# Kernel optimization log

Hardware: AMD Instinct MI355X
Metric: run time of the kernel (lower is better)

## Reference

```python
import jax, jax.numpy as jnp
import numpy as np

B = 8
H = W = 1280
STRIDES = (8, 16, 32)
TOP_K = 5000
CONF_TH = 0.3
NMS_TH = 0.3
KEEP_TOP_K = 750
NUM_KPS = 5


def _make_priors():
    # Mirrors _PriorBox: per feature cell [x, y, stride, stride] in pixels, offset=0,
    # x varies fastest (torch repeat pattern == row-major meshgrid 'xy').
    pts = []
    for s in STRIDES:
        fh, fw = H // s, W // s
        xs = np.arange(fw, dtype=np.float32) * s
        ys = np.arange(fh, dtype=np.float32) * s
        xx, yy = np.meshgrid(xs, ys)  # [fh, fw]
        p = np.stack([xx.ravel(), yy.ravel(),
                      np.full(fh * fw, s, np.float32),
                      np.full(fh * fw, s, np.float32)], axis=1)
        pts.append(p)
    return jnp.asarray(np.concatenate(pts, axis=0))  # [N, 4]


def setup_inputs() -> dict:
    key = jax.random.key(0)
    k1, k2, k3, k4 = jax.random.split(key, 4)
    priors = _make_priors()
    N = priors.shape[0]  # 33600
    return {
        'cls_preds': jax.random.uniform(k1, (B, N, 1), dtype=jnp.float32),
        'obj_preds': jax.random.uniform(k2, (B, N, 1), dtype=jnp.float32),
        'bbox_preds': jax.random.normal(k3, (B, N, 4), dtype=jnp.float32),
        'kps_preds': jax.random.normal(k4, (B, N, 2 * NUM_KPS), dtype=jnp.float32),
        'priors': priors,
    }


def _decode(bbox_preds, kps_preds, priors):
    # Faithful port of _decode with scale=1 (priors already in pixel units).
    pxy = priors[:, :2]   # [N,2]
    pwh = priors[:, 2:4]  # [N,2]
    cxy = pxy + bbox_preds[..., 0:2] * pwh                 # [B,N,2] box center
    wh = pwh * jnp.exp(bbox_preds[..., 2:4])               # [B,N,2] box size
    Bn, N = bbox_preds.shape[:2]
    kps = pxy[:, None, :] + kps_preds.reshape(Bn, N, NUM_KPS, 2) * pwh[:, None, :]
    x1y1 = cxy - wh * 0.5
    return jnp.concatenate([x1y1, x1y1 + wh, kps.reshape(Bn, N, 2 * NUM_KPS)], axis=-1)  # [B,N,14]


def _nms_keep(boxes, valid):
    # boxes: [K,4] xyxy sorted by score desc; valid: [K] bool. Greedy NMS keep mask.
    b = jax.lax.stop_gradient(boxes)
    area = jnp.maximum(b[:, 2] - b[:, 0], 0.0) * jnp.maximum(b[:, 3] - b[:, 1], 0.0)
    lt = jnp.maximum(b[:, None, :2], b[None, :, :2])
    rb = jnp.minimum(b[:, None, 2:], b[None, :, 2:])
    whi = jnp.maximum(rb - lt, 0.0)
    inter = whi[..., 0] * whi[..., 1]                      # [K,K]
    iou = inter / (area[:, None] + area[None, :] - inter + 1e-12)
    K = b.shape[0]
    jidx = jnp.arange(K)

    def body(i, keep):
        sup = keep[i] & (iou[i] > NMS_TH) & (jidx > i)
        return keep & ~sup

    return jax.lax.fori_loop(0, K, body, valid)


def reference(cls_preds, obj_preds, bbox_preds, kps_preds, priors):
    boxes = _decode(bbox_preds, kps_preds, priors)          # [B,N,14]
    scores = jnp.sqrt(cls_preds[..., 0] * obj_preds[..., 0])  # [B,N] geometric-mean score

    # confidence filter + pre-NMS top-k (masked scores sort invalids last)
    masked = jnp.where(scores > CONF_TH, scores, -1.0)
    top_scores, idx = jax.lax.top_k(masked, TOP_K)          # [B,K]
    top_boxes = jnp.take_along_axis(boxes, idx[..., None], axis=1)  # [B,K,14]
    valid = top_scores > CONF_TH

    keep = jax.lax.stop_gradient(jax.vmap(_nms_keep)(top_boxes[..., :4], valid))  # [B,K]

    dets = jnp.concatenate([top_boxes, top_scores[..., None]], axis=-1)  # [B,K,15]
    kept_scores = jnp.where(keep, top_scores, -1.0)
    fs, fidx = jax.lax.top_k(kept_scores, KEEP_TOP_K)
    out = jnp.take_along_axis(dets, fidx[..., None], axis=1)  # [B,750,15]
    out_valid = fs > CONF_TH                                   # [B,750]
    return out, out_valid
```

## Files before the change

kernel.cpp:

```cpp
#include <hip/hip_runtime.h>
#include <stdint.h>

#pragma clang fp contract(off)

static constexpr int TOPK  = 5000;
static constexpr int KEEPK = 750;
static constexpr int MPAD  = 65536;
static constexpr int NBLK  = (TOPK + 63) / 64;
static constexpr int KROW  = NBLK * 64;
static constexpr float TH  = 0.3f;

__device__ __forceinline__ uint32_t key_of(float f) {
  uint32_t u = __float_as_uint(f);
  u = (u & 0x80000000u) ? ~u : (u | 0x80000000u);
  return ~u;
}
__device__ __forceinline__ float val_of(uint32_t key) {
  uint32_t u = ~key;
  return (u & 0x80000000u) ? __uint_as_float(u ^ 0x80000000u) : __uint_as_float(~u);
}

__global__ void build_keys(const float* __restrict__ cls, const float* __restrict__ obj,
                           uint64_t* __restrict__ keys, int N) {
  int b = blockIdx.y;
  int i = blockIdx.x * blockDim.x + threadIdx.x;
  if (i >= MPAD) return;
  uint64_t c = ~0ull;
  if (i < N) {
    size_t o = (size_t)b * N + i;
    float s = sqrtf(cls[o] * obj[o]);
    float m = (s > TH) ? s : -1.0f;
    c = ((uint64_t)key_of(m) << 32) | (uint32_t)i;
  }
  keys[(size_t)b * MPAD + i] = c;
}

__global__ __launch_bounds__(1024) void bitonic_local_full(uint64_t* __restrict__ keys) {
  __shared__ uint64_t sh[8192];
  int base = blockIdx.x * 8192;
  uint64_t* a = keys + (size_t)blockIdx.y * MPAD + base;
  for (int t = threadIdx.x; t < 8192; t += 1024) sh[t] = a[t];
  __syncthreads();
  for (int k = 2; k <= 8192; k <<= 1) {
    for (int j = k >> 1; j > 0; j >>= 1) {
      for (int t = threadIdx.x; t < 4096; t += 1024) {
        int i = ((t & ~(j - 1)) << 1) | (t & (j - 1));
        int l = i | j;
        bool asc = (((base + i) & k) == 0);
        uint64_t x = sh[i], y = sh[l];
        if ((x > y) == asc) { sh[i] = y; sh[l] = x; }
      }
      __syncthreads();
    }
  }
  for (int t = threadIdx.x; t < 8192; t += 1024) a[t] = sh[t];
}

__global__ __launch_bounds__(1024) void merge_prune(const uint64_t* __restrict__ src,
                                                    uint64_t* __restrict__ dst) {
  __shared__ uint64_t sh[8192];
  int m = blockIdx.x, b = blockIdx.y;
  const uint64_t* A  = src + ((size_t)b * gridDim.x * 2 + 2 * m) * 8192;
  const uint64_t* Bp = A + 8192;
  for (int t = threadIdx.x; t < 8192; t += 1024) {
    uint64_t x = A[t], y = Bp[t];
    sh[t] = x < y ? x : y;
  }
  __syncthreads();
  bool asc = ((m & 1) == 0);
  for (int j = 4096; j > 0; j >>= 1) {
    for (int t = threadIdx.x; t < 4096; t += 1024) {
      int i = ((t & ~(j - 1)) << 1) | (t & (j - 1));
      int l = i | j;
      uint64_t x = sh[i], y = sh[l];
      if ((x > y) == asc) { sh[i] = y; sh[l] = x; }
    }
    __syncthreads();
  }
  uint64_t* D = dst + ((size_t)b * gridDim.x + m) * 8192;
  for (int t = threadIdx.x; t < 8192; t += 1024) D[t] = sh[t];
}

__global__ void gather_decode(const uint64_t* __restrict__ keys,
                              const float* __restrict__ bbox, const float* __restrict__ kps,
                              const float* __restrict__ priors,
                              float* __restrict__ dets, float* __restrict__ tscore, int N) {
  int b = blockIdx.y;
  int r = blockIdx.x * blockDim.x + threadIdx.x;
  if (r >= TOPK) return;
  uint64_t c = keys[(size_t)b * 8192 + r];
  uint32_t idx = (uint32_t)c;
  float score = val_of((uint32_t)(c >> 32));
  float4 pr = ((const float4*)priors)[idx];
  const float* bb = bbox + ((size_t)b * N + idx) * 4;
  float cx = pr.x + bb[0] * pr.z;
  float cy = pr.y + bb[1] * pr.w;
  float w = pr.z * expf(bb[2]);
  float h = pr.w * expf(bb[3]);
  float x1 = cx - w * 0.5f, y1 = cy - h * 0.5f;
  float* d = dets + ((size_t)b * TOPK + r) * 16;
  d[0] = x1; d[1] = y1; d[2] = x1 + w; d[3] = y1 + h;
  const float* kp = kps + ((size_t)b * N + idx) * 10;
#pragma unroll
  for (int q = 0; q < 5; ++q) {
    d[4 + 2 * q] = pr.x + kp[2 * q] * pr.z;
    d[5 + 2 * q] = pr.y + kp[2 * q + 1] * pr.w;
  }
  d[14] = score;
  tscore[(size_t)b * TOPK + r] = score;
}

__global__ __launch_bounds__(64) void nms_mask(const float* __restrict__ dets,
                                               uint64_t* __restrict__ tmask) {
  int sbk = blockIdx.x, tbk = blockIdx.y, b = blockIdx.z;
  if (tbk < sbk) return;
  __shared__ float4 tbox[64];
  int t = threadIdx.x;
  int j0 = tbk * 64;
  {
    int j = j0 + t;
    if (j < TOPK) {
      const float* dj = dets + ((size_t)b * TOPK + j) * 16;
      tbox[t] = make_float4(dj[0], dj[1], dj[2], dj[3]);
    } else tbox[t] = make_float4(0.f, 0.f, 0.f, 0.f);
  }
  __syncthreads();
  int i = sbk * 64 + t;
  uint64_t bits = 0;
  if (i < TOPK) {
    const float* di = dets + ((size_t)b * TOPK + i) * 16;
    float ix1 = di[0], iy1 = di[1], ix2 = di[2], iy2 = di[3];
    float iar = fmaxf(ix2 - ix1, 0.f) * fmaxf(iy2 - iy1, 0.f);
    int jmax = min(64, TOPK - j0);
    for (int u = 0; u < jmax; ++u) {
      int j = j0 + u;
      if (j <= i) continue;
      float4 bx = tbox[u];
      float xx1 = fmaxf(ix1, bx.x), yy1 = fmaxf(iy1, bx.y);
      float xx2 = fminf(ix2, bx.z), yy2 = fminf(iy2, bx.w);
      float ww = fmaxf(xx2 - xx1, 0.f), hh = fmaxf(yy2 - yy1, 0.f);
      float inter = ww * hh;
      float jar = fmaxf(bx.z - bx.x, 0.f) * fmaxf(bx.w - bx.y, 0.f);
      float iou = inter / (iar + jar - inter + 1e-12f);
      if (iou > TH) bits |= (1ull << u);
    }
  }
  uint64_t tw = 0;
#pragma unroll
  for (int u = 0; u < 64; ++u) {
    uint64_t bal = __ballot((bits >> u) & 1ull);
    if (t == u) tw = bal;
  }
  tmask[((size_t)b * NBLK + tbk) * KROW + (size_t)(sbk * 64 + t)] = tw;
}

__global__ __launch_bounds__(1024) void nms_fix_emit(const uint64_t* __restrict__ tmask,
                                                     const float* __restrict__ tscore,
                                                     const float* __restrict__ dets,
                                                     float* __restrict__ out, int B) {
  __shared__ uint64_t s_keep[2][80];
  __shared__ int s_changed;
  __shared__ int s_pref[NBLK + 1];
  int b = blockIdx.x;
  int tid = threadIdx.x;
  int wid = tid >> 6, lane = tid & 63;
  const uint64_t* mb = tmask + (size_t)b * NBLK * KROW;
  const float* sb = tscore + (size_t)b * TOPK;

  float sc[5];
  bool val[5];
#pragma unroll
  for (int q = 0; q < 5; ++q) {
    int j = tid + q * 1024;
    sc[q] = (j < TOPK) ? sb[j] : -1.0f;
    val[q] = (j < TOPK) && (sc[q] > TH);
  }
#pragma unroll
  for (int q = 0; q < 5; ++q) {
    uint64_t w = __ballot(val[q]);
    int ch = wid + q * 16;
    if (ch < NBLK && lane == 0) s_keep[0][ch] = w;
  }

  int cur = 0;
  for (;;) {
    __syncthreads();
    if (tid == 0) s_changed = 0;
    __syncthreads();
    const uint64_t* kp = s_keep[cur];
#pragma unroll
    for (int q = 0; q < 5; ++q) {
      int j = tid + q * 1024;
      int tc = j >> 6;
      uint64_t sup = 0;
      if (tc < NBLK) {
        const uint64_t* row = mb + (size_t)tc * KROW + lane;
        uint64_t a0 = 0, a1 = 0, a2 = 0, a3 = 0;
        int nw = tc + 1, w = 0;
        for (; w + 4 <= nw; w += 4) {
          uint64_t m0 = row[(w + 0) * 64], m1 = row[(w + 1) * 64];
          uint64_t m2 = row[(w + 2) * 64], m3 = row[(w + 3) * 64];
          a0 |= m0 & kp[w + 0]; a1 |= m1 & kp[w + 1];
          a2 |= m2 & kp[w + 2]; a3 |= m3 & kp[w + 3];
        }
        for (; w < nw; ++w) a0 |= row[w * 64] & kp[w];
        sup = (a0 | a1) | (a2 | a3);
      }
      uint64_t nk = __ballot(val[q] && sup == 0);
      int ch = wid + q * 16;
      if (ch < NBLK && lane == 0) {
        s_keep[cur ^ 1][ch] = nk;
        if (nk != kp[ch]) s_changed = 1;
      }
    }
    __syncthreads();
    if (!s_changed) break;
    cur ^= 1;
  }

  if (tid == 0) {
    int run = 0;
    for (int cb = 0; cb < NBLK; ++cb) { s_pref[cb] = run; run += __popcll(s_keep[cur][cb]); }
    s_pref[NBLK] = run;
  }
  __syncthreads();
  int K = s_pref[NBLK];

  for (int cb = wid; cb < NBLK; cb += 16) {
    int p = cb * 64 + lane;
    if (p >= TOPK) continue;
    uint64_t aw = s_keep[cur][cb];
    int kept = (int)((aw >> lane) & 1ull);
    int within = __popcll(aw & ((1ull << lane) - 1ull));
    int rank = s_pref[cb] + within;
    int slot = kept ? rank : (K + (p - s_pref[cb] - within));
    if (slot < KEEPK) {
      const float* d = dets + ((size_t)b * TOPK + p) * 16;
      float* o = out + ((size_t)b * KEEPK + slot) * 15;
#pragma unroll
      for (int ccol = 0; ccol < 15; ++ccol) o[ccol] = d[ccol];
      out[(size_t)B * KEEPK * 15 + (size_t)b * KEEPK + slot] = kept ? 1.0f : 0.0f;
    }
  }
}

extern "C" void kernel_launch(void* const* d_in, const int* in_sizes, int n_in,
                              void* d_out, int out_size, void* d_ws, size_t ws_size,
                              hipStream_t stream) {
  const float* cls    = (const float*)d_in[0];
  const float* obj    = (const float*)d_in[1];
  const float* bbox   = (const float*)d_in[2];
  const float* kps    = (const float*)d_in[3];
  const float* priors = (const float*)d_in[4];
  int N = in_sizes[4] / 4;
  int B = in_sizes[0] / N;
  if (N > MPAD) return;

  char* ws = (char*)d_ws;
  size_t off = 0;
  auto alloc = [&](size_t bytes) -> void* {
    void* p = ws + off;
    off += (bytes + 255) & ~(size_t)255;
    return p;
  };
  uint64_t* keys1  = (uint64_t*)alloc((size_t)B * MPAD * 8);
  float*    dets   = (float*)   alloc((size_t)B * TOPK * 16 * 4);
  float*    tscore = (float*)   alloc((size_t)B * TOPK * 4 + 4096);
  uint64_t* tmask  = (uint64_t*)alloc((size_t)B * NBLK * KROW * 8 + 4096);
  if (off > ws_size) return;
  uint64_t* keys2 = tmask;
  uint64_t* keys3 = keys2 + (size_t)B * 4 * 8192;
  uint64_t* keys4 = keys3 + (size_t)B * 2 * 8192;

  build_keys<<<dim3((MPAD + 255) / 256, B), 256, 0, stream>>>(cls, obj, keys1, N);
  bitonic_local_full<<<dim3(MPAD / 8192, B), 1024, 0, stream>>>(keys1);
  merge_prune<<<dim3(4, B), 1024, 0, stream>>>(keys1, keys2);
  merge_prune<<<dim3(2, B), 1024, 0, stream>>>(keys2, keys3);
  merge_prune<<<dim3(1, B), 1024, 0, stream>>>(keys3, keys4);
  gather_decode<<<dim3((TOPK + 255) / 256, B), 256, 0, stream>>>(keys4, bbox, kps, priors,
                                                                 dets, tscore, N);
  nms_mask<<<dim3(NBLK, NBLK, B), 64, 0, stream>>>(dets, tmask);
  nms_fix_emit<<<B, 1024, 0, stream>>>(tmask, tscore, dets, (float*)d_out, B);
}
```

Baseline: 377.5 us.

## Restructure NMS mask kernel: triangular grid, transposed loop, division-free IoU test

Launches only the upper-triangular block pairs through a linear pair index, so the grid no longer spawns blocks that exit immediately. Each thread now owns a target box and loops over source boxes held in shared memory, which produces the transposed mask word directly and removes the 64-step ballot transpose. The IoU threshold test becomes a multiply-compare against precomputed areas written by gather_decode, with an exact-division fallback for near-ties to keep bit-exactness. It costs an extra areas buffer, some integer sqrt math per block, and a slightly more complex diagonal mask.

After: 329.9 us. -12.6%, faster.

```diff
diff --git a/kernel.cpp b/kernel.cpp
--- a/kernel.cpp
+++ b/kernel.cpp
@@ -7,6 +7,7 @@
 static constexpr int KEEPK = 750;
 static constexpr int MPAD  = 65536;
 static constexpr int NBLK  = (TOPK + 63) / 64;
+static constexpr int NPAIR = NBLK * (NBLK + 1) / 2;
 static constexpr int KROW  = NBLK * 64;
 static constexpr float TH  = 0.3f;
 
@@ -84,7 +85,8 @@
 __global__ void gather_decode(const uint64_t* __restrict__ keys,
                               const float* __restrict__ bbox, const float* __restrict__ kps,
                               const float* __restrict__ priors,
-                              float* __restrict__ dets, float* __restrict__ tscore, int N) {
+                              float* __restrict__ dets, float* __restrict__ tscore,
+                              float* __restrict__ areas, int N) {
   int b = blockIdx.y;
   int r = blockIdx.x * blockDim.x + threadIdx.x;
   if (r >= TOPK) return;
@@ -98,8 +100,10 @@
   float w = pr.z * expf(bb[2]);
   float h = pr.w * expf(bb[3]);
   float x1 = cx - w * 0.5f, y1 = cy - h * 0.5f;
+  float x2 = x1 + w, y2 = y1 + h;
   float* d = dets + ((size_t)b * TOPK + r) * 16;
-  d[0] = x1; d[1] = y1; d[2] = x1 + w; d[3] = y1 + h;
+  d[0] = x1; d[1] = y1; d[2] = x2; d[3] = y2;
+  areas[(size_t)b * TOPK + r] = fmaxf(x2 - x1, 0.0f) * fmaxf(y2 - y1, 0.0f);
   const float* kp = kps + ((size_t)b * N + idx) * 10;
 #pragma unroll
   for (int q = 0; q < 5; ++q) {
@@ -111,46 +115,58 @@
 }
 
 __global__ __launch_bounds__(64) void nms_mask(const float* __restrict__ dets,
+                                               const float* __restrict__ areas,
                                                uint64_t* __restrict__ tmask) {
-  int sbk = blockIdx.x, tbk = blockIdx.y, b = blockIdx.z;
-  if (tbk < sbk) return;
-  __shared__ float4 tbox[64];
+  int pid = blockIdx.x, b = blockIdx.y;
+  int tbk = (int)((sqrtf(8.0f * (float)pid + 1.0f) - 1.0f) * 0.5f);
+  while (((tbk + 1) * (tbk + 2)) / 2 <= pid) ++tbk;
+  while ((tbk * (tbk + 1)) / 2 > pid) --tbk;
+  int sbk = pid - (tbk * (tbk + 1)) / 2;
+
+  __shared__ float4 sbox[64];
+  __shared__ float sarea[64];
   int t = threadIdx.x;
-  int j0 = tbk * 64;
   {
-    int j = j0 + t;
-    if (j < TOPK) {
-      const float* dj = dets + ((size_t)b * TOPK + j) * 16;
-      tbox[t] = make_float4(dj[0], dj[1], dj[2], dj[3]);
-    } else tbox[t] = make_float4(0.f, 0.f, 0.f, 0.f);
+    int i = min(sbk * 64 + t, TOPK - 1);
+    const float* di = dets + ((size_t)b * TOPK + i) * 16;
+    sbox[t] = make_float4(di[0], di[1], di[2], di[3]);
+    sarea[t] = areas[(size_t)b * TOPK + i];
   }
   __syncthreads();
-  int i = sbk * 64 + t;
-  uint64_t bits = 0;
-  if (i < TOPK) {
-    const float* di = dets + ((size_t)b * TOPK + i) * 16;
-    float ix1 = di[0], iy1 = di[1], ix2 = di[2], iy2 = di[3];
-    float iar = fmaxf(ix2 - ix1, 0.f) * fmaxf(iy2 - iy1, 0.f);
-    int jmax = min(64, TOPK - j0);
-    for (int u = 0; u < jmax; ++u) {
-      int j = j0 + u;
-      if (j <= i) continue;
-      float4 bx = tbox[u];
-      float xx1 = fmaxf(ix1, bx.x), yy1 = fmaxf(iy1, bx.y);
-      float xx2 = fminf(ix2, bx.z), yy2 = fminf(iy2, bx.w);
+
+  int jc = min(tbk * 64 + t, TOPK - 1);
+  const float* dj = dets + ((size_t)b * TOPK + jc) * 16;
+  float jx1 = dj[0], jy1 = dj[1], jx2 = dj[2], jy2 = dj[3];
+  float ja = areas[(size_t)b * TOPK + jc];
+
+  uint64_t tw = 0, unc = 0;
+#pragma unroll
+  for (int u = 0; u < 64; ++u) {
+    float4 bx = sbox[u];
+    float xx1 = fmaxf(jx1, bx.x), yy1 = fmaxf(jy1, bx.y);
+    float xx2 = fminf(jx2, bx.z), yy2 = fminf(jy2, bx.w);
+    float ww = fmaxf(xx2 - xx1, 0.f), hh = fmaxf(yy2 - yy1, 0.f);
+    float inter = ww * hh;
+    float denom = sarea[u] + ja - inter + 1e-12f;
+    float rhs = TH * denom;
+    tw  |= (uint64_t)(inter > rhs) << u;
+    unc |= (uint64_t)(fabsf(inter - rhs) <= 6e-7f * rhs) << u;
+  }
+  if (unc) {
+    do {
+      int u = __ffsll((unsigned long long)unc) - 1;
+      float4 bx = sbox[u];
+      float xx1 = fmaxf(jx1, bx.x), yy1 = fmaxf(jy1, bx.y);
+      float xx2 = fminf(jx2, bx.z), yy2 = fminf(jy2, bx.w);
       float ww = fmaxf(xx2 - xx1, 0.f), hh = fmaxf(yy2 - yy1, 0.f);
       float inter = ww * hh;
-      float jar = fmaxf(bx.z - bx.x, 0.f) * fmaxf(bx.w - bx.y, 0.f);
-      float iou = inter / (iar + jar - inter + 1e-12f);
-      if (iou > TH) bits |= (1ull << u);
-    }
-  }
-  uint64_t tw = 0;
-#pragma unroll
-  for (int u = 0; u < 64; ++u) {
-    uint64_t bal = __ballot((bits >> u) & 1ull);
-    if (t == u) tw = bal;
-  }
+      float denom = sarea[u] + ja - inter + 1e-12f;
+      uint64_t bit = 1ull << u;
+      tw = (tw & ~bit) | ((inter / denom > TH) ? bit : 0ull);
+      unc &= unc - 1;
+    } while (unc);
+  }
+  if (sbk == tbk) tw &= (t == 0) ? 0ull : ((1ull << t) - 1ull);
   tmask[((size_t)b * NBLK + tbk) * KROW + (size_t)(sbk * 64 + t)] = tw;
 }
 
@@ -266,6 +282,7 @@
   uint64_t* keys1  = (uint64_t*)alloc((size_t)B * MPAD * 8);
   float*    dets   = (float*)   alloc((size_t)B * TOPK * 16 * 4);
   float*    tscore = (float*)   alloc((size_t)B * TOPK * 4 + 4096);
+  float*    areas  = (float*)   alloc((size_t)B * TOPK * 4 + 4096);
   uint64_t* tmask  = (uint64_t*)alloc((size_t)B * NBLK * KROW * 8 + 4096);
   if (off > ws_size) return;
   uint64_t* keys2 = tmask;
@@ -278,7 +295,7 @@
   merge_prune<<<dim3(2, B), 1024, 0, stream>>>(keys2, keys3);
   merge_prune<<<dim3(1, B), 1024, 0, stream>>>(keys3, keys4);
   gather_decode<<<dim3((TOPK + 255) / 256, B), 256, 0, stream>>>(keys4, bbox, kps, priors,
-                                                                 dets, tscore, N);
-  nms_mask<<<dim3(NBLK, NBLK, B), 64, 0, stream>>>(dets, tmask);
+                                                                 dets, tscore, areas, N);
+  nms_mask<<<dim3(NPAIR, B), 64, 0, stream>>>(dets, areas, tmask);
   nms_fix_emit<<<B, 1024, 0, stream>>>(tmask, tscore, dets, (float*)d_out, B);
 }
```
